# Optimization experiments

Hardware: AMD Instinct MI355X
Metric: run time of the kernel (lower is better)

## Reference

```python
import jax, jax.numpy as jnp
import numpy as np

B, S, I = 32, 256, 256      # batch, seq_len, input_size
H, N, C, O = 512, 128, 64, 256  # lstm hidden, mem addresses, content bits, output
P = 4 * C + 12              # head params: read(k,beta,g,s3,gamma) + write(same + erase + add)
EPS = 1e-8


def setup_inputs() -> dict:
    key = jax.random.key(0)
    ks = jax.random.split(key, 8)
    sc = 0.05
    return {
        "inputs_BxSxI": jax.random.normal(ks[0], (B, S, I), jnp.float32),
        "W_ih": jax.random.normal(ks[1], (4 * H, I + C), jnp.float32) * sc,
        "W_hh": jax.random.normal(ks[2], (4 * H, H), jnp.float32) * sc,
        "b_lstm": jnp.zeros((4 * H,), jnp.float32),
        "W_head": jax.random.normal(ks[3], (P, H), jnp.float32) * sc,
        "b_head": jnp.zeros((P,), jnp.float32),
        "W_out": jax.random.normal(ks[4], (O, H + C), jnp.float32) * sc,
        "b_out": jnp.zeros((O,), jnp.float32),
    }


def _address(k, beta, g, s, gamma, w_prev, M):
    """NTM addressing: content (cosine sim * beta softmax) -> gate -> circular shift -> sharpen."""
    Mn = M / (jnp.linalg.norm(M, axis=-1, keepdims=True) + EPS)   # [B,N,C]
    kn = k / (jnp.linalg.norm(k, axis=-1, keepdims=True) + EPS)   # [B,C]
    wc = jax.nn.softmax(beta * jnp.einsum('bnc,bc->bn', Mn, kn), axis=-1)
    wg = g * wc + (1.0 - g) * w_prev                              # interpolation gate
    ws = (s[:, 0:1] * jnp.roll(wg, -1, axis=-1)                   # 3-tap circular conv shift
          + s[:, 1:2] * wg
          + s[:, 2:3] * jnp.roll(wg, 1, axis=-1))
    wp = (ws + EPS) ** gamma                                      # sharpening, gamma >= 1
    return wp / jnp.sum(wp, axis=-1, keepdims=True)


def _forward(x, W_ih, W_hh, b_lstm, W_head, b_head, W_out, b_out):
    Bv = x.shape[0]
    splits = np.cumsum([C, 1, 1, 3, 1, C, 1, 1, 3, 1, C]).tolist()

    def step(state, x_t):
        M, w_r, w_w, r, h, c = state
        # LSTM controller on [input, prev_read]
        gates = jnp.concatenate([x_t, r], -1) @ W_ih.T + h @ W_hh.T + b_lstm
        gi, gf, gg, go = jnp.split(gates, 4, axis=-1)
        c = jax.nn.sigmoid(gf) * c + jax.nn.sigmoid(gi) * jnp.tanh(gg)
        h = jax.nn.sigmoid(go) * jnp.tanh(c)
        # interface parameters
        p = h @ W_head.T + b_head
        (k_r, b_r, g_r, s_r, gm_r,
         k_w, b_w, g_w, s_w, gm_w, e_w, a_w) = jnp.split(p, splits, axis=-1)
        w_r = _address(k_r, jax.nn.softplus(b_r), jax.nn.sigmoid(g_r),
                       jax.nn.softmax(s_r, axis=-1), 1.0 + jax.nn.softplus(gm_r), w_r, M)
        w_w = _address(k_w, jax.nn.softplus(b_w), jax.nn.sigmoid(g_w),
                       jax.nn.softmax(s_w, axis=-1), 1.0 + jax.nn.softplus(gm_w), w_w, M)
        # write (erase then add), then read
        e = jax.nn.sigmoid(e_w)
        M = M * (1.0 - w_w[:, :, None] * e[:, None, :]) + w_w[:, :, None] * a_w[:, None, :]
        r = jnp.einsum('bn,bnc->bc', w_r, M)
        out = jnp.concatenate([h, r], -1) @ W_out.T + b_out
        return (M, w_r, w_w, r, h, c), out

    w0 = jnp.zeros((Bv, N), jnp.float32).at[:, 0].set(1.0)
    init = (jnp.full((Bv, N, C), 0.01, jnp.float32), w0, w0,
            jnp.zeros((Bv, C), jnp.float32),
            jnp.zeros((Bv, H), jnp.float32), jnp.zeros((Bv, H), jnp.float32))
    _, outs = jax.lax.scan(step, init, jnp.swapaxes(x, 0, 1))  # [S,B,O]
    return jnp.swapaxes(outs, 0, 1)                            # [B,S,O]


def reference(inputs_BxSxI, W_ih, W_hh, b_lstm, W_head, b_head, W_out, b_out):
    return _forward(inputs_BxSxI, W_ih, W_hh, b_lstm, W_head, b_head, W_out, b_out)
```

## Files before the change

### kernel.cpp

```cpp
#include <hip/hip_runtime.h>
#include <hip/hip_fp16.h>
#include <math.h>

#define B_  32
#define S_  256
#define I_  256
#define H_  512
#define N_  128
#define C_  64
#define O_  256
#define P_  268
#define K_  832
#define HB  (H_*B_)
#define EPSX 1e-8f
#define NBLK 160
#define NPB  32

#define OFF_XT   0
#define SZ_XT    (S_*I_*B_)
#define OFF_HA   (OFF_XT + SZ_XT)
#define SZ_HA    ((S_+1)*H_*B_)
#define OFF_RA   (OFF_HA + SZ_HA)
#define SZ_RA    ((S_+1)*C_*B_)
#define OFF_CT   (OFF_RA + SZ_RA)
#define SZ_CT    (H_*B_)
#define OFF_M    (OFF_CT + SZ_CT)
#define SZ_M     (B_*N_*C_)
#define OFF_WR   (OFF_M + SZ_M)
#define SZ_W     (B_*N_)
#define OFF_WW   (OFF_WR + SZ_W)
#define OFF_BAR  (OFF_WW + SZ_W)
#define SZ_BAR   8192
#define OFF_WOT  (OFF_BAR + SZ_BAR)
#define SZ_WOT   ((H_+C_)*O_)
#define OFF_WHH  (OFF_WOT + SZ_WOT)
#define SZ_WHH   ((P_*H_)/2)

__device__ __forceinline__ float sigm(float x) { return 1.f / (1.f + expf(-x)); }
__device__ __forceinline__ float splus(float x) {
    return fmaxf(x, 0.f) + log1pf(expf(-fabsf(x)));
}
__device__ __forceinline__ float wave_max(float v) {
    #pragma unroll
    for (int s = 1; s < 64; s <<= 1) v = fmaxf(v, __shfl_xor(v, s, 64));
    return v;
}
__device__ __forceinline__ float wave_sum(float v) {
    #pragma unroll
    for (int s = 1; s < 64; s <<= 1) v += __shfl_xor(v, s, 64);
    return v;
}

__device__ __forceinline__ void junk16(float& s) {
    #pragma unroll
    for (int d = 0; d < 16; ++d) s = fmaf(s, 1.0000001f, 1e-9f);
    asm volatile("" : "+v"(s));
}

__device__ __forceinline__ void hotwait(unsigned* p, unsigned tgt) {
    float s = 1.f;
    while (__hip_atomic_load(p, __ATOMIC_RELAXED, __HIP_MEMORY_SCOPE_AGENT) < tgt)
        junk16(s);
}

__device__ __forceinline__ void gbar(unsigned* bar, volatile unsigned* ldsf,
                                     int bi, int tid, unsigned seq)
{
    __syncthreads();
    if (bi == NBLK - 1) {
        if (tid < NBLK - 1) hotwait(&bar[tid * 16], seq);
        else {
            float s = 1.f;
            junk16(s);
        }
        __syncthreads();
        if (tid < NBLK)
            __hip_atomic_store(&bar[4096 + tid * 16], seq, __ATOMIC_RELAXED,
                               __HIP_MEMORY_SCOPE_AGENT);
        __syncthreads();
    } else {
        if (tid == 0) {
            asm volatile("s_waitcnt vmcnt(0) lgkmcnt(0)" ::: "memory");
            __hip_atomic_store(&bar[bi * 16], seq, __ATOMIC_RELAXED,
                               __HIP_MEMORY_SCOPE_AGENT);
        }
        float s = (float)(tid + 1);
        for (;;) {
            if (*ldsf >= seq) break;
            if (tid == 0 &&
                __hip_atomic_load(&bar[4096 + bi * 16], __ATOMIC_RELAXED,
                                  __HIP_MEMORY_SCOPE_AGENT) >= seq)
                *ldsf = seq;
            junk16(s);
        }
        __syncthreads();
    }
}

__global__ __launch_bounds__(256)
void prep_kernel(const float* __restrict__ x, const float* __restrict__ Wout,
                 const float* __restrict__ Whead, float* __restrict__ ws)
{
    int g = blockIdx.x * 256 + threadIdx.x;
    if (g < SZ_XT) {
        int b = g & 31, k = (g >> 5) & 255, t = g >> 13;
        ws[OFF_XT + g] = x[b * (S_*I_) + t * I_ + k];
        return;
    }
    g -= SZ_XT;
    if (g < SZ_WOT) {
        int o = g & 255, k = g >> 8;
        ws[OFF_WOT + g] = Wout[o * (H_ + C_) + k];
        return;
    }
    g -= SZ_WOT;
    if (g < HB)      { ws[OFF_HA + g] = 0.f;   return; }
    g -= HB;
    if (g < C_*B_)   { ws[OFF_RA + g] = 0.f;   return; }
    g -= C_*B_;
    if (g < SZ_CT)   { ws[OFF_CT + g] = 0.f;   return; }
    g -= SZ_CT;
    if (g < SZ_M)    { ws[OFF_M  + g] = 0.01f; return; }
    g -= SZ_M;
    if (g < 2*SZ_W)  { ws[OFF_WR + g] = 0.f;   return; }
    g -= 2*SZ_W;
    if (g < SZ_BAR)  { ws[OFF_BAR + g] = 0.f;  return; }
    g -= SZ_BAR;
    if (g < P_ * H_) {
        ((__half*)(ws + OFF_WHH))[g] = __float2half(Whead[g]);
        return;
    }
}

#define GEMM_STEP(khat, ap) {                                             \
    const float4 a0 = *(const float4*)(ap);                               \
    const float4 a1 = *(const float4*)((ap) + 4);                         \
    const float2 w01 = *(const float2*)&Wt[(khat) * 18 + (rg << 2)];      \
    const float2 w23 = *(const float2*)&Wt[(khat) * 18 + (rg << 2) + 2];  \
    const float wv[4] = {w01.x, w01.y, w23.x, w23.y};                     \
    const float av[8] = {a0.x, a0.y, a0.z, a0.w, a1.x, a1.y, a1.z, a1.w}; \
    _Pragma("unroll")                                                     \
    for (int j = 0; j < 4; ++j)                                           \
        _Pragma("unroll")                                                 \
        for (int bb = 0; bb < 8; ++bb)                                    \
            acc[j][bb] += wv[j] * av[bb]; }

__global__ __launch_bounds__(512)
void ntm_loop(const float* __restrict__ Wih, const float* __restrict__ Whh,
              const float* __restrict__ bl,  const float* __restrict__ bhead,
              float* __restrict__ ws)
{
    float* xT  = ws + OFF_XT;
    float* hA  = ws + OFF_HA;
    float* rA  = ws + OFF_RA;
    float* Mem = ws + OFF_M;
    unsigned* bar = (unsigned*)(ws + OFF_BAR);
    const unsigned short* whH = (const unsigned short*)(ws + OFF_WHH);

    __shared__ float Wt[K_ * 18];
    __shared__ float p_lds[P_];
    __shared__ float wldsR[128];
    __shared__ float wldsW[128];
    __shared__ float h_lds[H_];
    __shared__ unsigned relf;

    const int tid  = threadIdx.x;
    const int bi   = blockIdx.x;
    const bool isPB = (bi < NPB);
    const int gi   = bi - NPB;

    if (tid == 0) relf = 0;

    if (!isPB) {
        for (int idx = tid; idx < K_ * 16; idx += 512) {
            int rl = idx & 15, k = idx >> 4;
            int row = (rl & 3) * H_ + gi * 4 + (rl >> 2);
            float v = (k < I_ + C_) ? Wih[row * (I_ + C_) + k]
                                    : Whh[row * H_ + (k - (I_ + C_))];
            Wt[k * 18 + rl] = v;
        }
    } else if (tid < N_) {
        wldsR[tid] = (tid == 0) ? 1.f : 0.f;
        wldsW[tid] = (tid == 0) ? 1.f : 0.f;
    }
    __syncthreads();

    const int pair = tid >> 5;
    const int ks   = tid & 31;
    const int rg   = pair >> 2;
    const int bg   = pair & 3;
    const int b0   = bg * 8;

    float acc[4][8];
    float cr[8] = {0,0,0,0,0,0,0,0};
    float bI = 0, bF = 0, bG = 0, bO = 0;
    if (!isPB && ks == 0) {
        const int unit = gi * 4 + rg;
        bI = bl[unit];        bF = bl[H_ + unit];
        bG = bl[2*H_ + unit]; bO = bl[3*H_ + unit];
    }

    if (!isPB) {
        #pragma unroll
        for (int j = 0; j < 4; ++j)
            #pragma unroll
            for (int bb = 0; bb < 8; ++bb) acc[j][bb] = 0.f;
        {
            const float* xs = xT;
            const float* hs = hA;
            #pragma unroll
            for (int i = 0; i < 8; ++i) {
                const int k = ks + (i << 5);
                GEMM_STEP(k, xs + k * B_ + b0);
            }
            #pragma unroll
            for (int i = 0; i < 16; ++i) {
                const int k = ks + (i << 5);
                GEMM_STEP(320 + k, hs + k * B_ + b0);
            }
        }
    }

    unsigned seq = 0;

    for (int t = 0; t < S_; ++t) {
        if (!isPB) {
            const float* rs = rA + (size_t)t * C_ * B_;
            #pragma unroll
            for (int i = 0; i < 2; ++i) {
                const int k = ks + (i << 5);
                GEMM_STEP(256 + k, rs + k * B_ + b0);
            }
            #pragma unroll
            for (int j = 0; j < 4; ++j)
                #pragma unroll
                for (int bb = 0; bb < 8; ++bb) {
                    float v = acc[j][bb];
                    v += __shfl_xor(v, 16, 64);
                    v += __shfl_xor(v, 8, 64);
                    v += __shfl_xor(v, 4, 64);
                    v += __shfl_xor(v, 2, 64);
                    v += __shfl_xor(v, 1, 64);
                    acc[j][bb] = v;
                }
            if (ks == 0) {
                const int unit = gi * 4 + rg;
                #pragma unroll
                for (int bb = 0; bb < 8; ++bb) {
                    const int b = b0 + bb;
                    float gI = acc[0][bb] + bI;
                    float gF = acc[1][bb] + bF;
                    float gG = acc[2][bb] + bG;
                    float gO = acc[3][bb] + bO;
                    float cN = sigm(gF) * cr[bb] + sigm(gI) * tanhf(gG);
                    float hN = sigm(gO) * tanhf(cN);
                    cr[bb] = cN;
                    __hip_atomic_store(&hA[(size_t)(t + 1) * HB + unit * B_ + b],
                                       hN, __ATOMIC_RELAXED,
                                       __HIP_MEMORY_SCOPE_AGENT);
                }
            }
        }
        gbar(bar, &relf, bi, tid, ++seq);

        if (isPB) {
            const int b = bi;
            float* Mb = Mem + (size_t)b * N_ * C_;
            const float* hs = hA + (size_t)(t + 1) * HB;

            h_lds[tid] = __hip_atomic_load(&hs[tid * B_ + b], __ATOMIC_RELAXED,
                                           __HIP_MEMORY_SCOPE_AGENT);
            __syncthreads();

            {
                const int sub  = tid & 1;
                const int row0 = tid >> 1;
                const float* hb = &h_lds[sub * 256];
                #pragma unroll
                for (int rep = 0; rep < 2; ++rep) {
                    const int row = (rep == 0) ? row0
                                  : ((row0 < P_ - 256) ? row0 + 256 : -1);
                    if (row >= 0) {
                        const unsigned short* wrow = whH + row * H_ + sub * 256;
                        float acch = 0.f;
                        #pragma unroll 4
                        for (int k2 = 0; k2 < 256; k2 += 8) {
                            float4 raw = *(const float4*)&wrow[k2];
                            const __half2* hp = (const __half2*)&raw;
                            float2 f0 = __half22float2(hp[0]);
                            float2 f1 = __half22float2(hp[1]);
                            float2 f2 = __half22float2(hp[2]);
                            float2 f3 = __half22float2(hp[3]);
                            acch += f0.x * hb[k2]     + f0.y * hb[k2 + 1]
                                  + f1.x * hb[k2 + 2] + f1.y * hb[k2 + 3]
                                  + f2.x * hb[k2 + 4] + f2.y * hb[k2 + 5]
                                  + f3.x * hb[k2 + 6] + f3.y * hb[k2 + 7];
                        }
                        acch += __shfl_xor(acch, 1, 64);
                        if (sub == 0) p_lds[row] = acch + bhead[row];
                    }
                }
            }
            __syncthreads();

            {
                float* wtmpA = h_lds;
                float* sbufA = h_lds + 256;
                const int grp = (tid >> 7) & 1;
                const int l   = tid & 127;
                const bool act256 = (tid < 256);
                const int o = grp ? 70 : 0;
                const int widx = (tid >> 6) & 1;

                float z = 0.f, gate = 0.f, s0 = 0.f, s1 = 0.f, s2 = 0.f,
                      gamma = 1.f;
                if (act256) {
                    float beta = splus(p_lds[o + 64]);
                    gate = sigm(p_lds[o + 65]);
                    float sa = p_lds[o + 66], sbv = p_lds[o + 67],
                          sc = p_lds[o + 68];
                    float sm3 = fmaxf(sa, fmaxf(sbv, sc));
                    float ea = __expf(sa - sm3), eb = __expf(sbv - sm3),
                          ec = __expf(sc - sm3);
                    float es3 = ea + eb + ec;
                    s0 = ea / es3; s1 = eb / es3; s2 = ec / es3;
                    gamma = 1.f + splus(p_lds[o + 69]);
                    float kk = 0.f;
                    #pragma unroll 8
                    for (int c = 0; c < C_; ++c) {
                        float kv = p_lds[o + c]; kk += kv * kv;
                    }
                    const float knorm = sqrtf(kk) + EPSX;
                    float dot = 0.f, mm = 0.f;
                    #pragma unroll
                    for (int c = 0; c < C_; c += 4) {
                        float4 m4 = *(const float4*)&Mb[l * C_ + c];
                        dot += m4.x * p_lds[o + c]     + m4.y * p_lds[o + c + 1]
                             + m4.z * p_lds[o + c + 2] + m4.w * p_lds[o + c + 3];
                        mm  += m4.x * m4.x + m4.y * m4.y + m4.z * m4.z
                             + m4.w * m4.w;
                    }
                    z = beta * (dot / ((sqrtf(mm) + EPSX) * knorm));
                }
                float zm = wave_max(z);
                if (act256 && (tid & 63) == 0) sbufA[grp * 8 + widx] = zm;
                __syncthreads();
                const float zmax = fmaxf(sbufA[grp * 8], sbufA[grp * 8 + 1]);
                float ev = act256 ? __expf(z - zmax) : 0.f;
                float es = wave_sum(ev);
                if (act256 && (tid & 63) == 0) sbufA[grp * 8 + 2 + widx] = es;
                __syncthreads();
                const float esum = sbufA[grp * 8 + 2] + sbufA[grp * 8 + 3];
                if (act256) {
                    float wc = ev / esum;
                    float wprev = grp ? wldsW[l] : wldsR[l];
                    wtmpA[grp * 128 + l] = gate * wc + (1.f - gate) * wprev;
                }
                __syncthreads();
                float wp = 0.f;
                if (act256) {
                    float wsft = s0 * wtmpA[grp * 128 + ((l + 1) & 127)]
                               + s1 * wtmpA[grp * 128 + l]
                               + s2 * wtmpA[grp * 128 + ((l - 1) & 127)];
                    wp = __powf(wsft + EPSX, gamma);
                }
                float ps = wave_sum(wp);
                if (act256 && (tid & 63) == 0) sbufA[grp * 8 + 4 + widx] = ps;
                __syncthreads();
                const float psum = sbufA[grp * 8 + 4] + sbufA[grp * 8 + 5];
                if (act256) {
                    float wn = wp / psum;
                    if (grp) wldsW[l] = wn; else wldsR[l] = wn;
                }
                __syncthreads();
            }

            for (int idx = tid; idx < (N_ * C_) / 4; idx += 512) {
                const int n = idx >> 4;
                const int c = (idx & 15) << 2;
                const float wwn = wldsW[n];
                float4 m4 = *(float4*)&Mb[n * C_ + c];
                m4.x = m4.x * (1.f - wwn * sigm(p_lds[140 + c]))     + wwn * p_lds[204 + c];
                m4.y = m4.y * (1.f - wwn * sigm(p_lds[140 + c + 1])) + wwn * p_lds[204 + c + 1];
                m4.z = m4.z * (1.f - wwn * sigm(p_lds[140 + c + 2])) + wwn * p_lds[204 + c + 2];
                m4.w = m4.w * (1.f - wwn * sigm(p_lds[140 + c + 3])) + wwn * p_lds[204 + c + 3];
                *(float4*)&Mb[n * C_ + c] = m4;
            }
            __syncthreads();

            {
                const int c = tid >> 3, ns = tid & 7;
                float accr = 0.f;
                #pragma unroll
                for (int i = 0; i < 16; ++i) {
                    const int n = ns + 8 * i;
                    accr += wldsR[n] * Mb[n * C_ + c];
                }
                accr += __shfl_xor(accr, 4, 64);
                accr += __shfl_xor(accr, 2, 64);
                accr += __shfl_xor(accr, 1, 64);
                if (ns == 0)
                    __hip_atomic_store(&rA[(size_t)(t + 1) * C_ * B_ + c * B_ + b],
                                       accr, __ATOMIC_RELAXED,
                                       __HIP_MEMORY_SCOPE_AGENT);
            }
        } else {
            #pragma unroll
            for (int j = 0; j < 4; ++j)
                #pragma unroll
                for (int bb = 0; bb < 8; ++bb) acc[j][bb] = 0.f;
            if (t + 1 < S_) {
                const float* xs = xT + (size_t)(t + 1) * I_ * B_;
                const float* hs = hA + (size_t)(t + 1) * HB;
                #pragma unroll
                for (int i = 0; i < 8; ++i) {
                    const int k = ks + (i << 5);
                    GEMM_STEP(k, xs + k * B_ + b0);
                }
                #pragma unroll
                for (int i = 0; i < 16; ++i) {
                    const int k = ks + (i << 5);
                    GEMM_STEP(320 + k, hs + k * B_ + b0);
                }
            }
        }
        gbar(bar, &relf, bi, tid, ++seq);
    }
}

__global__ __launch_bounds__(256)
void out_kernel(const float* __restrict__ ws, const float* __restrict__ bout,
                float* __restrict__ out)
{
    __shared__ float actL[(H_ + C_) * 16];
    const float* hA  = ws + OFF_HA;
    const float* rA  = ws + OFF_RA;
    const float* WoT = ws + OFF_WOT;
    const int t   = blockIdx.x >> 1;
    const int bh  = blockIdx.x & 1;
    const int tid = threadIdx.x;

    for (int idx = tid; idx < (H_ + C_) * 16; idx += 256) {
        const int k = idx >> 4, bl2 = idx & 15, b = bh * 16 + bl2;
        float v = (k < H_) ? hA[(size_t)(t + 1) * HB + k * B_ + b]
                           : rA[(size_t)(t + 1) * C_ * B_ + (k - H_) * B_ + b];
        actL[k * 16 + bl2] = v;
    }
    __syncthreads();

    const int ot = tid & 63, bt = tid >> 6;
    const int o0 = ot * 4, bl0 = bt * 4;
    float acc[4][4] = {{0,0,0,0},{0,0,0,0},{0,0,0,0},{0,0,0,0}};
    for (int k = 0; k < H_ + C_; ++k) {
        const float4 w4 = *(const float4*)&WoT[k * O_ + o0];
        const float4 a4 = *(const float4*)&actL[k * 16 + bl0];
        const float wv[4] = {w4.x, w4.y, w4.z, w4.w};
        const float av[4] = {a4.x, a4.y, a4.z, a4.w};
        #pragma unroll
        for (int j = 0; j < 4; ++j)
            #pragma unroll
            for (int bb = 0; bb < 4; ++bb)
                acc[j][bb] += wv[j] * av[bb];
    }
    const float4 bo = *(const float4*)&bout[o0];
    #pragma unroll
    for (int bb = 0; bb < 4; ++bb) {
        const int b = bh * 16 + bl0 + bb;
        float4 res;
        res.x = acc[0][bb] + bo.x;
        res.y = acc[1][bb] + bo.y;
        res.z = acc[2][bb] + bo.z;
        res.w = acc[3][bb] + bo.w;
        *(float4*)&out[((size_t)b * S_ + t) * O_ + o0] = res;
    }
}

extern "C" void kernel_launch(void* const* d_in, const int* in_sizes, int n_in,
                              void* d_out, int out_size, void* d_ws, size_t ws_size,
                              hipStream_t stream)
{
    const float* x    = (const float*)d_in[0];
    const float* Wih  = (const float*)d_in[1];
    const float* Whh  = (const float*)d_in[2];
    const float* bl   = (const float*)d_in[3];
    const float* Whd  = (const float*)d_in[4];
    const float* bhd  = (const float*)d_in[5];
    const float* Wout = (const float*)d_in[6];
    const float* bout = (const float*)d_in[7];
    float* ws  = (float*)d_ws;
    float* out = (float*)d_out;

    prep_kernel<<<10529, 256, 0, stream>>>(x, Wout, Whd, ws);

    void* args[] = { (void*)&Wih, (void*)&Whh, (void*)&bl,
                     (void*)&bhd, (void*)&ws };
    (void)hipLaunchCooperativeKernel((void*)ntm_loop, dim3(NBLK), dim3(512), args, 0, stream);

    out_kernel<<<512, 256, 0, stream>>>(ws, bout, out);
}
```

Measured before the change: 7.902 ms.

## Replace centralized grid barrier with producer-consumer flag waits between gate and memory blocks

Drops the two-phase global barrier coordinated by the last block and gives each role its own progress flags. Gate blocks publish h-ready flags and wait only on the 32 memory blocks' r-ready flags, while memory blocks wait on all 128 gate flags. Each block polls the flags directly with wave-wide __all checks instead of going through a master block, which removes one relay hop per barrier and lets the gate blocks' next-step GEMM start without a full grid rendezvous. The cost is more polling traffic from many blocks reading many flags, and correctness now depends on the flag ordering and memory fences.

```diff
diff --git a/kernel.cpp b/kernel.cpp
--- a/kernel.cpp
+++ b/kernel.cpp
@@ -15,6 +15,7 @@
 #define EPSX 1e-8f
 #define NBLK 160
 #define NPB  32
+#define NGATE 128
 
 #define OFF_XT   0
 #define SZ_XT    (S_*I_*B_)
@@ -57,44 +58,27 @@
     asm volatile("" : "+v"(s));
 }
 
-__device__ __forceinline__ void hotwait(unsigned* p, unsigned tgt) {
-    float s = 1.f;
-    while (__hip_atomic_load(p, __ATOMIC_RELAXED, __HIP_MEMORY_SCOPE_AGENT) < tgt)
-        junk16(s);
-}
-
-__device__ __forceinline__ void gbar(unsigned* bar, volatile unsigned* ldsf,
-                                     int bi, int tid, unsigned seq)
+__device__ __forceinline__ void wait_flags(unsigned* flags, int nf, unsigned tgt,
+                                           volatile unsigned* ldsp, int tid)
 {
+    const int wv = tid >> 6, ln = tid & 63;
+    if (wv < 2) {
+        int idx = wv * 64 + ln;
+        if (idx >= nf) idx = nf - 1;
+        unsigned* p = &flags[idx * 16];
+        float s = 1.f;
+        for (;;) {
+            unsigned v = __hip_atomic_load(p, __ATOMIC_RELAXED,
+                                           __HIP_MEMORY_SCOPE_AGENT);
+            if (__all((int)(v >= tgt))) break;
+            junk16(s);
+        }
+        if (ln == 0) ldsp[wv] = tgt;
+    } else {
+        float s = (float)(tid + 1);
+        while (ldsp[0] < tgt || ldsp[1] < tgt) junk16(s);
+    }
     __syncthreads();
-    if (bi == NBLK - 1) {
-        if (tid < NBLK - 1) hotwait(&bar[tid * 16], seq);
-        else {
-            float s = 1.f;
-            junk16(s);
-        }
-        __syncthreads();
-        if (tid < NBLK)
-            __hip_atomic_store(&bar[4096 + tid * 16], seq, __ATOMIC_RELAXED,
-                               __HIP_MEMORY_SCOPE_AGENT);
-        __syncthreads();
-    } else {
-        if (tid == 0) {
-            asm volatile("s_waitcnt vmcnt(0) lgkmcnt(0)" ::: "memory");
-            __hip_atomic_store(&bar[bi * 16], seq, __ATOMIC_RELAXED,
-                               __HIP_MEMORY_SCOPE_AGENT);
-        }
-        float s = (float)(tid + 1);
-        for (;;) {
-            if (*ldsf >= seq) break;
-            if (tid == 0 &&
-                __hip_atomic_load(&bar[4096 + bi * 16], __ATOMIC_RELAXED,
-                                  __HIP_MEMORY_SCOPE_AGENT) >= seq)
-                *ldsf = seq;
-            junk16(s);
-        }
-        __syncthreads();
-    }
 }
 
 __global__ __launch_bounds__(256)
@@ -155,6 +139,8 @@
     float* rA  = ws + OFF_RA;
     float* Mem = ws + OFF_M;
     unsigned* bar = (unsigned*)(ws + OFF_BAR);
+    unsigned* flag_h = bar;
+    unsigned* flag_r = bar + 4096;
     const unsigned short* whH = (const unsigned short*)(ws + OFF_WHH);
 
     __shared__ float Wt[K_ * 18];
@@ -162,14 +148,14 @@
     __shared__ float wldsR[128];
     __shared__ float wldsW[128];
     __shared__ float h_lds[H_];
-    __shared__ unsigned relf;
+    __shared__ unsigned syncf[4];
 
     const int tid  = threadIdx.x;
     const int bi   = blockIdx.x;
     const bool isPB = (bi < NPB);
     const int gi   = bi - NPB;
 
-    if (tid == 0) relf = 0;
+    if (tid < 4) syncf[tid] = 0;
 
     if (!isPB) {
         for (int idx = tid; idx < K_ * 16; idx += 512) {
@@ -205,26 +191,22 @@
         for (int j = 0; j < 4; ++j)
             #pragma unroll
             for (int bb = 0; bb < 8; ++bb) acc[j][bb] = 0.f;
-        {
-            const float* xs = xT;
-            const float* hs = hA;
-            #pragma unroll
-            for (int i = 0; i < 8; ++i) {
-                const int k = ks + (i << 5);
-                GEMM_STEP(k, xs + k * B_ + b0);
-            }
-            #pragma unroll
-            for (int i = 0; i < 16; ++i) {
-                const int k = ks + (i << 5);
-                GEMM_STEP(320 + k, hs + k * B_ + b0);
-            }
-        }
-    }
-
-    unsigned seq = 0;
-
-    for (int t = 0; t < S_; ++t) {
-        if (!isPB) {
+        const float* xs = xT;
+        const float* hs = hA;
+        #pragma unroll
+        for (int i = 0; i < 8; ++i) {
+            const int k = ks + (i << 5);
+            GEMM_STEP(k, xs + k * B_ + b0);
+        }
+        #pragma unroll
+        for (int i = 0; i < 16; ++i) {
+            const int k = ks + (i << 5);
+            GEMM_STEP(320 + k, hs + k * B_ + b0);
+        }
+
+        for (int t = 0; t < S_; ++t) {
+            wait_flags(flag_r, NPB, (unsigned)t, &syncf[0], tid);
+
             const float* rs = rA + (size_t)t * C_ * B_;
             #pragma unroll
             for (int i = 0; i < 2; ++i) {
@@ -260,171 +242,184 @@
                                        __HIP_MEMORY_SCOPE_AGENT);
                 }
             }
-        }
-        gbar(bar, &relf, bi, tid, ++seq);
-
-        if (isPB) {
-            const int b = bi;
-            float* Mb = Mem + (size_t)b * N_ * C_;
-            const float* hs = hA + (size_t)(t + 1) * HB;
-
-            h_lds[tid] = __hip_atomic_load(&hs[tid * B_ + b], __ATOMIC_RELAXED,
-                                           __HIP_MEMORY_SCOPE_AGENT);
-            __syncthreads();
-
-            {
-                const int sub  = tid & 1;
-                const int row0 = tid >> 1;
-                const float* hb = &h_lds[sub * 256];
-                #pragma unroll
-                for (int rep = 0; rep < 2; ++rep) {
-                    const int row = (rep == 0) ? row0
-                                  : ((row0 < P_ - 256) ? row0 + 256 : -1);
-                    if (row >= 0) {
-                        const unsigned short* wrow = whH + row * H_ + sub * 256;
-                        float acch = 0.f;
-                        #pragma unroll 4
-                        for (int k2 = 0; k2 < 256; k2 += 8) {
-                            float4 raw = *(const float4*)&wrow[k2];
-                            const __half2* hp = (const __half2*)&raw;
-                            float2 f0 = __half22float2(hp[0]);
-                            float2 f1 = __half22float2(hp[1]);
-                            float2 f2 = __half22float2(hp[2]);
-                            float2 f3 = __half22float2(hp[3]);
-                            acch += f0.x * hb[k2]     + f0.y * hb[k2 + 1]
-                                  + f1.x * hb[k2 + 2] + f1.y * hb[k2 + 3]
-                                  + f2.x * hb[k2 + 4] + f2.y * hb[k2 + 5]
-                                  + f3.x * hb[k2 + 6] + f3.y * hb[k2 + 7];
-                        }
-                        acch += __shfl_xor(acch, 1, 64);
-                        if (sub == 0) p_lds[row] = acch + bhead[row];
-                    }
-                }
-            }
-            __syncthreads();
-
-            {
-                float* wtmpA = h_lds;
-                float* sbufA = h_lds + 256;
-                const int grp = (tid >> 7) & 1;
-                const int l   = tid & 127;
-                const bool act256 = (tid < 256);
-                const int o = grp ? 70 : 0;
-                const int widx = (tid >> 6) & 1;
-
-                float z = 0.f, gate = 0.f, s0 = 0.f, s1 = 0.f, s2 = 0.f,
-                      gamma = 1.f;
-                if (act256) {
-                    float beta = splus(p_lds[o + 64]);
-                    gate = sigm(p_lds[o + 65]);
-                    float sa = p_lds[o + 66], sbv = p_lds[o + 67],
-                          sc = p_lds[o + 68];
-                    float sm3 = fmaxf(sa, fmaxf(sbv, sc));
-                    float ea = __expf(sa - sm3), eb = __expf(sbv - sm3),
-                          ec = __expf(sc - sm3);
-                    float es3 = ea + eb + ec;
-                    s0 = ea / es3; s1 = eb / es3; s2 = ec / es3;
-                    gamma = 1.f + splus(p_lds[o + 69]);
-                    float kk = 0.f;
-                    #pragma unroll 8
-                    for (int c = 0; c < C_; ++c) {
-                        float kv = p_lds[o + c]; kk += kv * kv;
-                    }
-                    const float knorm = sqrtf(kk) + EPSX;
-                    float dot = 0.f, mm = 0.f;
-                    #pragma unroll
-                    for (int c = 0; c < C_; c += 4) {
-                        float4 m4 = *(const float4*)&Mb[l * C_ + c];
-                        dot += m4.x * p_lds[o + c]     + m4.y * p_lds[o + c + 1]
-                             + m4.z * p_lds[o + c + 2] + m4.w * p_lds[o + c + 3];
-                        mm  += m4.x * m4.x + m4.y * m4.y + m4.z * m4.z
-                             + m4.w * m4.w;
-                    }
-                    z = beta * (dot / ((sqrtf(mm) + EPSX) * knorm));
-                }
-                float zm = wave_max(z);
-                if (act256 && (tid & 63) == 0) sbufA[grp * 8 + widx] = zm;
-                __syncthreads();
-                const float zmax = fmaxf(sbufA[grp * 8], sbufA[grp * 8 + 1]);
-                float ev = act256 ? __expf(z - zmax) : 0.f;
-                float es = wave_sum(ev);
-                if (act256 && (tid & 63) == 0) sbufA[grp * 8 + 2 + widx] = es;
-                __syncthreads();
-                const float esum = sbufA[grp * 8 + 2] + sbufA[grp * 8 + 3];
-                if (act256) {
-                    float wc = ev / esum;
-                    float wprev = grp ? wldsW[l] : wldsR[l];
-                    wtmpA[grp * 128 + l] = gate * wc + (1.f - gate) * wprev;
-                }
-                __syncthreads();
-                float wp = 0.f;
-                if (act256) {
-                    float wsft = s0 * wtmpA[grp * 128 + ((l + 1) & 127)]
-                               + s1 * wtmpA[grp * 128 + l]
-                               + s2 * wtmpA[grp * 128 + ((l - 1) & 127)];
-                    wp = __powf(wsft + EPSX, gamma);
-                }
-                float ps = wave_sum(wp);
-                if (act256 && (tid & 63) == 0) sbufA[grp * 8 + 4 + widx] = ps;
-                __syncthreads();
-                const float psum = sbufA[grp * 8 + 4] + sbufA[grp * 8 + 5];
-                if (act256) {
-                    float wn = wp / psum;
-                    if (grp) wldsW[l] = wn; else wldsR[l] = wn;
-                }
-                __syncthreads();
-            }
-
-            for (int idx = tid; idx < (N_ * C_) / 4; idx += 512) {
-                const int n = idx >> 4;
-                const int c = (idx & 15) << 2;
-                const float wwn = wldsW[n];
-                float4 m4 = *(float4*)&Mb[n * C_ + c];
-                m4.x = m4.x * (1.f - wwn * sigm(p_lds[140 + c]))     + wwn * p_lds[204 + c];
-                m4.y = m4.y * (1.f - wwn * sigm(p_lds[140 + c + 1])) + wwn * p_lds[204 + c + 1];
-                m4.z = m4.z * (1.f - wwn * sigm(p_lds[140 + c + 2])) + wwn * p_lds[204 + c + 2];
-                m4.w = m4.w * (1.f - wwn * sigm(p_lds[140 + c + 3])) + wwn * p_lds[204 + c + 3];
-                *(float4*)&Mb[n * C_ + c] = m4;
-            }
-            __syncthreads();
-
-            {
-                const int c = tid >> 3, ns = tid & 7;
-                float accr = 0.f;
-                #pragma unroll
-                for (int i = 0; i < 16; ++i) {
-                    const int n = ns + 8 * i;
-                    accr += wldsR[n] * Mb[n * C_ + c];
-                }
-                accr += __shfl_xor(accr, 4, 64);
-                accr += __shfl_xor(accr, 2, 64);
-                accr += __shfl_xor(accr, 1, 64);
-                if (ns == 0)
-                    __hip_atomic_store(&rA[(size_t)(t + 1) * C_ * B_ + c * B_ + b],
-                                       accr, __ATOMIC_RELAXED,
-                                       __HIP_MEMORY_SCOPE_AGENT);
-            }
-        } else {
+            __syncthreads();
+            if (tid == 0) {
+                asm volatile("s_waitcnt vmcnt(0) lgkmcnt(0)" ::: "memory");
+                __hip_atomic_store(&flag_h[gi * 16], (unsigned)(t + 1),
+                                   __ATOMIC_RELAXED, __HIP_MEMORY_SCOPE_AGENT);
+            }
+            wait_flags(flag_h, NGATE, (unsigned)(t + 1), &syncf[2], tid);
+
             #pragma unroll
             for (int j = 0; j < 4; ++j)
                 #pragma unroll
                 for (int bb = 0; bb < 8; ++bb) acc[j][bb] = 0.f;
             if (t + 1 < S_) {
-                const float* xs = xT + (size_t)(t + 1) * I_ * B_;
-                const float* hs = hA + (size_t)(t + 1) * HB;
+                const float* xs2 = xT + (size_t)(t + 1) * I_ * B_;
+                const float* hs2 = hA + (size_t)(t + 1) * HB;
                 #pragma unroll
                 for (int i = 0; i < 8; ++i) {
                     const int k = ks + (i << 5);
-                    GEMM_STEP(k, xs + k * B_ + b0);
+                    GEMM_STEP(k, xs2 + k * B_ + b0);
                 }
                 #pragma unroll
                 for (int i = 0; i < 16; ++i) {
                     const int k = ks + (i << 5);
-                    GEMM_STEP(320 + k, hs + k * B_ + b0);
-                }
-            }
-        }
-        gbar(bar, &relf, bi, tid, ++seq);
+                    GEMM_STEP(320 + k, hs2 + k * B_ + b0);
+                }
+            }
+        }
+        return;
+    }
+
+    const int b = bi;
+    float* Mb = Mem + (size_t)b * N_ * C_;
+    for (int t = 0; t < S_; ++t) {
+        wait_flags(flag_h, NGATE, (unsigned)(t + 1), &syncf[0], tid);
+
+        const float* hs = hA + (size_t)(t + 1) * HB;
+        h_lds[tid] = __hip_atomic_load(&hs[tid * B_ + b], __ATOMIC_RELAXED,
+                                       __HIP_MEMORY_SCOPE_AGENT);
+        __syncthreads();
+
+        {
+            const int sub  = tid & 1;
+            const int row0 = tid >> 1;
+            const float* hb = &h_lds[sub * 256];
+            #pragma unroll
+            for (int rep = 0; rep < 2; ++rep) {
+                const int row = (rep == 0) ? row0
+                              : ((row0 < P_ - 256) ? row0 + 256 : -1);
+                if (row >= 0) {
+                    const unsigned short* wrow = whH + row * H_ + sub * 256;
+                    float acch = 0.f;
+                    #pragma unroll 4
+                    for (int k2 = 0; k2 < 256; k2 += 8) {
+                        float4 raw = *(const float4*)&wrow[k2];
+                        const __half2* hp = (const __half2*)&raw;
+                        float2 f0 = __half22float2(hp[0]);
+                        float2 f1 = __half22float2(hp[1]);
+                        float2 f2 = __half22float2(hp[2]);
+                        float2 f3 = __half22float2(hp[3]);
+                        acch += f0.x * hb[k2]     + f0.y * hb[k2 + 1]
+                              + f1.x * hb[k2 + 2] + f1.y * hb[k2 + 3]
+                              + f2.x * hb[k2 + 4] + f2.y * hb[k2 + 5]
+                              + f3.x * hb[k2 + 6] + f3.y * hb[k2 + 7];
+                    }
+                    acch += __shfl_xor(acch, 1, 64);
+                    if (sub == 0) p_lds[row] = acch + bhead[row];
+                }
+            }
+        }
+        __syncthreads();
+
+        {
+            float* wtmpA = h_lds;
+            float* sbufA = h_lds + 256;
+            const int grp = (tid >> 7) & 1;
+            const int l   = tid & 127;
+            const bool act256 = (tid < 256);
+            const int o = grp ? 70 : 0;
+            const int widx = (tid >> 6) & 1;
+
+            float z = 0.f, gate = 0.f, s0 = 0.f, s1 = 0.f, s2 = 0.f,
+                  gamma = 1.f;
+            if (act256) {
+                float beta = splus(p_lds[o + 64]);
+                gate = sigm(p_lds[o + 65]);
+                float sa = p_lds[o + 66], sbv = p_lds[o + 67],
+                      sc = p_lds[o + 68];
+                float sm3 = fmaxf(sa, fmaxf(sbv, sc));
+                float ea = __expf(sa - sm3), eb = __expf(sbv - sm3),
+                      ec = __expf(sc - sm3);
+                float es3 = ea + eb + ec;
+                s0 = ea / es3; s1 = eb / es3; s2 = ec / es3;
+                gamma = 1.f + splus(p_lds[o + 69]);
+                float kk = 0.f;
+                #pragma unroll 8
+                for (int c = 0; c < C_; ++c) {
+                    float kv = p_lds[o + c]; kk += kv * kv;
+                }
+                const float knorm = sqrtf(kk) + EPSX;
+                float dot = 0.f, mm = 0.f;
+                #pragma unroll
+                for (int c = 0; c < C_; c += 4) {
+                    float4 m4 = *(const float4*)&Mb[l * C_ + c];
+                    dot += m4.x * p_lds[o + c]     + m4.y * p_lds[o + c + 1]
+                         + m4.z * p_lds[o + c + 2] + m4.w * p_lds[o + c + 3];
+                    mm  += m4.x * m4.x + m4.y * m4.y + m4.z * m4.z
+                         + m4.w * m4.w;
+                }
+                z = beta * (dot / ((sqrtf(mm) + EPSX) * knorm));
+            }
+            float zm = wave_max(z);
+            if (act256 && (tid & 63) == 0) sbufA[grp * 8 + widx] = zm;
+            __syncthreads();
+            const float zmax = fmaxf(sbufA[grp * 8], sbufA[grp * 8 + 1]);
+            float ev = act256 ? __expf(z - zmax) : 0.f;
+            float es = wave_sum(ev);
+            if (act256 && (tid & 63) == 0) sbufA[grp * 8 + 2 + widx] = es;
+            __syncthreads();
+            const float esum = sbufA[grp * 8 + 2] + sbufA[grp * 8 + 3];
+            if (act256) {
+                float wc = ev / esum;
+                float wprev = grp ? wldsW[l] : wldsR[l];
+                wtmpA[grp * 128 + l] = gate * wc + (1.f - gate) * wprev;
+            }
+            __syncthreads();
+            float wp = 0.f;
+            if (act256) {
+                float wsft = s0 * wtmpA[grp * 128 + ((l + 1) & 127)]
+                           + s1 * wtmpA[grp * 128 + l]
+                           + s2 * wtmpA[grp * 128 + ((l - 1) & 127)];
+                wp = __powf(wsft + EPSX, gamma);
+            }
+            float ps = wave_sum(wp);
+            if (act256 && (tid & 63) == 0) sbufA[grp * 8 + 4 + widx] = ps;
+            __syncthreads();
+            const float psum = sbufA[grp * 8 + 4] + sbufA[grp * 8 + 5];
+            if (act256) {
+                float wn = wp / psum;
+                if (grp) wldsW[l] = wn; else wldsR[l] = wn;
+            }
+            __syncthreads();
+        }
+
+        for (int idx = tid; idx < (N_ * C_) / 4; idx += 512) {
+            const int n = idx >> 4;
+            const int c = (idx & 15) << 2;
+            const float wwn = wldsW[n];
+            float4 m4 = *(float4*)&Mb[n * C_ + c];
+            m4.x = m4.x * (1.f - wwn * sigm(p_lds[140 + c]))     + wwn * p_lds[204 + c];
+            m4.y = m4.y * (1.f - wwn * sigm(p_lds[140 + c + 1])) + wwn * p_lds[204 + c + 1];
+            m4.z = m4.z * (1.f - wwn * sigm(p_lds[140 + c + 2])) + wwn * p_lds[204 + c + 2];
+            m4.w = m4.w * (1.f - wwn * sigm(p_lds[140 + c + 3])) + wwn * p_lds[204 + c + 3];
+            *(float4*)&Mb[n * C_ + c] = m4;
+        }
+        __syncthreads();
+
+        {
+            const int c = tid >> 3, ns = tid & 7;
+            float accr = 0.f;
+            #pragma unroll
+            for (int i = 0; i < 16; ++i) {
+                const int n = ns + 8 * i;
+                accr += wldsR[n] * Mb[n * C_ + c];
+            }
+            accr += __shfl_xor(accr, 4, 64);
+            accr += __shfl_xor(accr, 2, 64);
+            accr += __shfl_xor(accr, 1, 64);
+            if (ns == 0)
+                __hip_atomic_store(&rA[(size_t)(t + 1) * C_ * B_ + c * B_ + b],
+                                   accr, __ATOMIC_RELAXED,
+                                   __HIP_MEMORY_SCOPE_AGENT);
+        }
+        __syncthreads();
+        if (tid == 0) {
+            asm volatile("s_waitcnt vmcnt(0) lgkmcnt(0)" ::: "memory");
+            __hip_atomic_store(&flag_r[b * 16], (unsigned)(t + 1),
+                               __ATOMIC_RELAXED, __HIP_MEMORY_SCOPE_AGENT);
+        }
     }
 }
 
```

Result: faster. 7.115 ms (-10.0%).
